# Kernel optimization log

Measured on AMD Instinct MI355X. Metric: run time of the kernel, lower is better.

Reference implementation:

```python
import jax, jax.numpy as jnp
import numpy as np

B, T, H = 2, 2048, 1024
EXPAND, N = 2, 16
DIN = H * EXPAND  # 2048
EPS = 1e-6


def rmsnorm(x, w):
    var = jnp.mean(x * x, axis=-1, keepdims=True)
    return x * jax.lax.rsqrt(var + EPS) * w


def setup_inputs() -> dict:
    key = jax.random.key(0)
    ks = jax.random.split(key, 9)
    s_h = 1.0 / np.sqrt(H)
    s_d = 1.0 / np.sqrt(DIN)
    return {
        "x": jax.random.normal(ks[0], (B, T, H), jnp.float32),
        "norm_w": jnp.ones((H,), jnp.float32),
        "in_proj_w": jax.random.normal(ks[1], (H, 2 * DIN), jnp.float32) * s_h,
        "A_proj_w": jax.random.normal(ks[2], (DIN, DIN), jnp.float32) * s_d,
        "A_proj_b": jax.random.normal(ks[3], (DIN,), jnp.float32) * 0.02,
        "A_base": jnp.log(jnp.arange(1, N + 1, dtype=jnp.float32)),
        "B_proj_w": jax.random.normal(ks[4], (DIN, N), jnp.float32) * s_d,
        "C_proj_w": jax.random.normal(ks[5], (DIN, N), jnp.float32) * s_d,
        "D": jnp.ones((DIN,), jnp.float32),
        "out_proj_w": jax.random.normal(ks[6], (DIN, H), jnp.float32) * s_d,
    }


def liquid_scan(x_in, a_mod, a_base, B_in, C_in):
    # x_in, a_mod: [B,T,DIN]; B_in, C_in: [B,T,N]; a_base: [N]
    def step(h, inp):
        a_t, b_t, c_t, x_t = inp  # [B,DIN], [B,N], [B,N], [B,DIN]
        # h: [B, DIN, N]
        h = (a_t[:, :, None] * a_base) * h + b_t[:, None, :] * x_t[:, :, None]
        y_t = jnp.einsum('bdn,bn->bd', h, c_t)
        return h, y_t

    h0 = jnp.zeros((x_in.shape[0], DIN, N), x_in.dtype)
    xs = (jnp.swapaxes(a_mod, 0, 1), jnp.swapaxes(B_in, 0, 1),
          jnp.swapaxes(C_in, 0, 1), jnp.swapaxes(x_in, 0, 1))
    _, ys = jax.lax.scan(step, h0, xs)  # ys: [T,B,DIN]
    return jnp.swapaxes(ys, 0, 1)


def reference(x, norm_w, in_proj_w, A_proj_w, A_proj_b, A_base, B_proj_w, C_proj_w, D, out_proj_w):
    residual = x
    xn = rmsnorm(x, norm_w)
    xz = xn @ in_proj_w                      # [B,T,2*DIN]
    x_in, z = jnp.split(xz, 2, axis=-1)
    x_in = jax.nn.silu(x_in)
    a_mod = jax.nn.sigmoid(x_in @ A_proj_w + A_proj_b)  # [B,T,DIN]
    a_base = jax.nn.sigmoid(A_base)                      # [N]
    B_in = x_in @ B_proj_w                               # [B,T,N]
    C_in = x_in @ C_proj_w                               # [B,T,N]
    y = liquid_scan(x_in, a_mod, a_base, B_in, C_in)     # [B,T,DIN]
    y = (y + D * x_in) * jax.nn.silu(z)
    return residual + y @ out_proj_w
```

## Files before the change

### kernel.cpp

```cpp
#include <hip/hip_runtime.h>
#include <hip/hip_fp16.h>
#include <cstdint>

#define B_    2
#define T_    2048
#define H_    1024
#define DIN_  2048
#define NS_   16
#define M_    (B_*T_)
#define NCHUNK 32
#define LCHUNK 64

using bf16x8 = __attribute__((ext_vector_type(8))) short;
using f32x4  = __attribute__((ext_vector_type(4))) float;

__device__ __forceinline__ unsigned short f2bf(float f) {
    union { float f; uint32_t u; } x; x.f = f;
    uint32_t u = x.u;
    uint32_t r = (u + 0x7fffu + ((u >> 16) & 1u)) >> 16;
    return (unsigned short)r;
}
__device__ __forceinline__ float bf2f(unsigned short h) {
    union { uint32_t u; float f; } x; x.u = ((uint32_t)h) << 16;
    return x.f;
}
__device__ __forceinline__ float sigm(float v) { return 1.0f / (1.0f + expf(-v)); }
__device__ __forceinline__ float silu(float v) { return v / (1.0f + expf(-v)); }

__device__ __forceinline__ void gload_lds16(const void* g, void* l) {
    __builtin_amdgcn_global_load_lds(
        (__attribute__((address_space(1))) void*)(void*)g,
        (__attribute__((address_space(3))) void*)l, 16, 0, 0);
}

__global__ __launch_bounds__(256)
void prep_weights(const float* __restrict__ in_proj, const float* __restrict__ A_proj,
                  const float* __restrict__ B_proj, const float* __restrict__ C_proj,
                  const float* __restrict__ out_proj,
                  unsigned short* __restrict__ inT, unsigned short* __restrict__ W2,
                  unsigned short* __restrict__ outT) {
    int bid = blockIdx.x;
    int tid = threadIdx.x;
    if (bid >= 10240) {
        int l = bid - 10240;
        const float* src = (l < 64) ? B_proj : C_proj;
        int rowoff = (l < 64) ? 2048 : 2064;
        int k0 = (l & 63) * 32;
        int r = tid >> 4, c = tid & 15;
#pragma unroll
        for (int rr = 0; rr < 32; rr += 16) {
            float v = src[(size_t)(k0 + r + rr) * 16 + c];
            W2[(size_t)(rowoff + c) * 2048 + (k0 + r + rr)] = f2bf(v);
        }
        return;
    }
    const float* src; unsigned short* dst; int K, N, l;
    if (bid < 4096)      { src = in_proj;  dst = inT;  K = 1024; N = 4096; l = bid; }
    else if (bid < 8192) { src = A_proj;   dst = W2;   K = 2048; N = 2048; l = bid - 4096; }
    else                 { src = out_proj; dst = outT; K = 2048; N = 1024; l = bid - 8192; }
    int ntiles = N >> 5;
    int n0 = (l % ntiles) * 32, k0 = (l / ntiles) * 32;
    __shared__ float tile[32][33];
    int tx = tid & 31, ty = tid >> 5;
#pragma unroll
    for (int i = 0; i < 32; i += 8)
        tile[ty + i][tx] = src[(size_t)(k0 + ty + i) * N + (n0 + tx)];
    __syncthreads();
    int sx = (tid & 15) * 2;
    int sy = tid >> 4;
#pragma unroll
    for (int i = 0; i < 32; i += 16) {
        int n = sy + i;
        float v0 = tile[sx][n], v1 = tile[sx + 1][n];
        size_t o = (size_t)(n0 + n) * K + (k0 + sx);
        *(ushort2*)&dst[o] = make_ushort2(f2bf(v0), f2bf(v1));
    }
}

__global__ __launch_bounds__(256)
void rmsnorm_bf(const float* __restrict__ x, const float* __restrict__ w,
                unsigned short* __restrict__ xh) {
    int row = blockIdx.x;
    int tid = threadIdx.x;
    const float4* xr = (const float4*)(x + (size_t)row * H_);
    float4 v = xr[tid];
    float ss = v.x * v.x + v.y * v.y + v.z * v.z + v.w * v.w;
#pragma unroll
    for (int o = 32; o > 0; o >>= 1) ss += __shfl_down(ss, o, 64);
    __shared__ float red[4];
    int lane = tid & 63, wv = tid >> 6;
    if (lane == 0) red[wv] = ss;
    __syncthreads();
    float tot = red[0] + red[1] + red[2] + red[3];
    float rstd = rsqrtf(tot / (float)H_ + 1e-6f);
    const float4* wr = (const float4*)w;
    float4 w4 = wr[tid];
    size_t o = (size_t)row * H_ + tid * 4;
    *(ushort4*)&xh[o] = make_ushort4(f2bf(v.x * rstd * w4.x), f2bf(v.y * rstd * w4.y),
                                     f2bf(v.z * rstd * w4.z), f2bf(v.w * rstd * w4.w));
}

template <int EPI, int TM>
__global__ __launch_bounds__(256)
void gemm_bf(const unsigned short* __restrict__ Aa, const unsigned short* __restrict__ Bw,
             int K,
             float* __restrict__ out0,
             unsigned short* __restrict__ oh, unsigned short* __restrict__ oz,
             const float* __restrict__ aux,
             __half* __restrict__ oha, float* __restrict__ obin, float* __restrict__ ocin) {
    constexpr int UA    = TM / 16;
    constexpr int UNITS = UA + 8;
    constexpr int SPW   = UNITS / 4;
    constexpr int WM    = TM / 32;
    __shared__ unsigned short sm[3][UNITS * 512];
    const int tid  = threadIdx.x;
    const int lane = tid & 63;
    const int wid  = tid >> 6;
    const int wm   = wid >> 1, wn = wid & 1;

    const int gx   = gridDim.x;
    const int nwg  = gx * gridDim.y;
    const int orig = blockIdx.y * gx + blockIdx.x;
    const int qq   = nwg >> 3;
    const int lid  = (orig & 7) * qq + (orig >> 3);
    const int bm   = (lid / gx) * TM;
    const int bn   = (lid % gx) * 128;

    const unsigned short* b0 = Aa + (size_t)bm * K;
    const unsigned short* b1 = Bw + (size_t)bn * K;
    const int srow  = lane >> 2;
    const int sgran = (lane & 3) ^ ((lane >> 3) & 3);
    const unsigned short* gp[SPW];
    int lofs[SPW];
#pragma unroll
    for (int j = 0; j < SPW; ++j) {
        int u = wid * SPW + j;
        const unsigned short* base = (u < UA) ? b0 : b1;
        int chunk = (u < UA) ? u : (u - UA);
        gp[j] = base + (size_t)(chunk * 16 + srow) * K + sgran * 8;
        lofs[j] = u * 512;
    }

    const int nk = K >> 5;
#pragma unroll
    for (int j = 0; j < SPW; ++j) gload_lds16(gp[j], &sm[0][lofs[j]]);
#pragma unroll
    for (int j = 0; j < SPW; ++j) gload_lds16(gp[j] + 32, &sm[1][lofs[j]]);

    const int fro = (lane & 15) * 32 + (((lane >> 4) ^ ((lane >> 1) & 3)) * 8);

    f32x4 acc[WM][4] = {};
    int bsel = 0;
    for (int kt = 0; kt < nk; ++kt) {
        if (kt + 1 < nk) {
            if constexpr (SPW == 4) asm volatile("s_waitcnt vmcnt(4)" ::: "memory");
            else                    asm volatile("s_waitcnt vmcnt(3)" ::: "memory");
        } else {
            asm volatile("s_waitcnt vmcnt(0)" ::: "memory");
        }
        __builtin_amdgcn_s_barrier();
        __builtin_amdgcn_sched_barrier(0);
        if (kt + 2 < nk) {
            int nb = bsel + 2; if (nb >= 3) nb -= 3;
#pragma unroll
            for (int j = 0; j < SPW; ++j)
                gload_lds16(gp[j] + (kt + 2) * 32, &sm[nb][lofs[j]]);
        }
        const unsigned short* sb = sm[bsel];
        bf16x8 af[WM], bf8[4];
#pragma unroll
        for (int m = 0; m < WM; ++m)
            af[m] = *(const bf16x8*)&sb[(wm * WM + m) * 512 + fro];
#pragma unroll
        for (int n = 0; n < 4; ++n)
            bf8[n] = *(const bf16x8*)&sb[(UA + wn * 4 + n) * 512 + fro];
#pragma unroll
        for (int m = 0; m < WM; ++m)
#pragma unroll
            for (int n = 0; n < 4; ++n)
                acc[m][n] = __builtin_amdgcn_mfma_f32_16x16x32_bf16(af[m], bf8[n], acc[m][n], 0, 0, 0);
        bsel += 1; if (bsel == 3) bsel = 0;
    }

#pragma unroll
    for (int m = 0; m < WM; ++m)
#pragma unroll
        for (int n = 0; n < 4; ++n) {
            int col  = bn + wn * 64 + n * 16 + (lane & 15);
            int row0 = bm + wm * (WM * 16) + m * 16 + ((lane >> 4) << 2);
#pragma unroll
            for (int r = 0; r < 4; ++r) {
                int row = row0 + r;
                float v = acc[m][n][r];
                if (EPI == 0) {
                    float s = silu(v);
                    if (col < DIN_) oh[(size_t)row * DIN_ + col] = f2bf(s);
                    else            oz[(size_t)row * DIN_ + (col - DIN_)] = f2bf(s);
                } else if (EPI == 1) {
                    if (col < 2048)      oha[(size_t)row * DIN_ + col] = __float2half(sigm(v + aux[col]));
                    else if (col < 2064) obin[(size_t)row * 16 + (col - 2048)] = v;
                    else if (col < 2080) ocin[(size_t)row * 16 + (col - 2064)] = v;
                } else {
                    out0[(size_t)row * H_ + col] = v + aux[(size_t)row * H_ + col];
                }
            }
        }
}

__global__ __launch_bounds__(256)
void scan_phase1(const __half* __restrict__ amod, const unsigned short* __restrict__ xh,
                 const float* __restrict__ Bin, const float* __restrict__ Abase,
                 float* __restrict__ P, float* __restrict__ S) {
    int d = blockIdx.x * 256 + threadIdx.x;
    int c = blockIdx.y;
    int b = blockIdx.z;
    float ab[16];
#pragma unroll
    for (int n = 0; n < 16; ++n) ab[n] = sigm(Abase[n]);
    float p[16], s[16];
#pragma unroll
    for (int n = 0; n < 16; ++n) { p[n] = 1.0f; s[n] = 0.0f; }
    int t0 = c * LCHUNK;
    for (int tt = 0; tt < LCHUNK; ++tt) {
        size_t mrow = (size_t)(b * T_ + t0 + tt);
        float a = __half2float(amod[mrow * DIN_ + d]);
        float x = bf2f(xh[mrow * DIN_ + d]);
        const float4* bt4 = (const float4*)(Bin + mrow * 16);
        float4 q0 = bt4[0], q1 = bt4[1], q2 = bt4[2], q3 = bt4[3];
        float bt[16];
        bt[0]=q0.x; bt[1]=q0.y; bt[2]=q0.z; bt[3]=q0.w;
        bt[4]=q1.x; bt[5]=q1.y; bt[6]=q1.z; bt[7]=q1.w;
        bt[8]=q2.x; bt[9]=q2.y; bt[10]=q2.z; bt[11]=q2.w;
        bt[12]=q3.x; bt[13]=q3.y; bt[14]=q3.z; bt[15]=q3.w;
#pragma unroll
        for (int n = 0; n < 16; ++n) {
            float dk = a * ab[n];
            p[n] *= dk;
            s[n] = fmaf(dk, s[n], bt[n] * x);
        }
    }
    size_t base = ((size_t)(b * NCHUNK + c) << 15) + (size_t)d * 16;
    float4* P4 = (float4*)(P + base);
    float4* S4 = (float4*)(S + base);
#pragma unroll
    for (int j = 0; j < 4; ++j) {
        P4[j] = make_float4(p[4*j], p[4*j+1], p[4*j+2], p[4*j+3]);
        S4[j] = make_float4(s[4*j], s[4*j+1], s[4*j+2], s[4*j+3]);
    }
}

__global__ __launch_bounds__(256)
void scan_phase2(const float* __restrict__ P, const float* __restrict__ S,
                 float* __restrict__ H0) {
    int idx = blockIdx.x * 256 + threadIdx.x;
    int b = idx >> 15;
    int dn = idx & 32767;
    float g = 0.f;
    for (int c = 0; c < NCHUNK; ++c) {
        size_t base = ((size_t)(b * NCHUNK + c) << 15) + dn;
        H0[base] = g;
        g = fmaf(P[base], g, S[base]);
    }
}

__global__ __launch_bounds__(256)
void scan_phase3(const __half* __restrict__ amod, const unsigned short* __restrict__ xh,
                 const float* __restrict__ Bin, const float* __restrict__ Cin,
                 const float* __restrict__ Abase, const float* __restrict__ H0,
                 const float* __restrict__ Dp, const unsigned short* __restrict__ szh,
                 unsigned short* __restrict__ yh) {
    int d = blockIdx.x * 256 + threadIdx.x;
    int c = blockIdx.y;
    int b = blockIdx.z;
    float ab[16];
#pragma unroll
    for (int n = 0; n < 16; ++n) ab[n] = sigm(Abase[n]);
    float h[16];
    size_t hbase = ((size_t)(b * NCHUNK + c) << 15) + (size_t)d * 16;
    const float4* H4 = (const float4*)(H0 + hbase);
#pragma unroll
    for (int j = 0; j < 4; ++j) {
        float4 t4 = H4[j];
        h[j*4] = t4.x; h[j*4+1] = t4.y; h[j*4+2] = t4.z; h[j*4+3] = t4.w;
    }
    float Dd = Dp[d];
    int t0 = c * LCHUNK;
    for (int tt = 0; tt < LCHUNK; ++tt) {
        size_t mrow = (size_t)(b * T_ + t0 + tt);
        float a = __half2float(amod[mrow * DIN_ + d]);
        float x = bf2f(xh[mrow * DIN_ + d]);
        const float4* bt4 = (const float4*)(Bin + mrow * 16);
        const float4* ct4 = (const float4*)(Cin + mrow * 16);
        float4 q0 = bt4[0], q1 = bt4[1], q2 = bt4[2], q3 = bt4[3];
        float4 r0 = ct4[0], r1 = ct4[1], r2 = ct4[2], r3 = ct4[3];
        float bt[16], ct[16];
        bt[0]=q0.x; bt[1]=q0.y; bt[2]=q0.z; bt[3]=q0.w;
        bt[4]=q1.x; bt[5]=q1.y; bt[6]=q1.z; bt[7]=q1.w;
        bt[8]=q2.x; bt[9]=q2.y; bt[10]=q2.z; bt[11]=q2.w;
        bt[12]=q3.x; bt[13]=q3.y; bt[14]=q3.z; bt[15]=q3.w;
        ct[0]=r0.x; ct[1]=r0.y; ct[2]=r0.z; ct[3]=r0.w;
        ct[4]=r1.x; ct[5]=r1.y; ct[6]=r1.z; ct[7]=r1.w;
        ct[8]=r2.x; ct[9]=r2.y; ct[10]=r2.z; ct[11]=r2.w;
        ct[12]=r3.x; ct[13]=r3.y; ct[14]=r3.z; ct[15]=r3.w;
        float y = 0.f;
#pragma unroll
        for (int n = 0; n < 16; ++n) {
            float dk = a * ab[n];
            h[n] = fmaf(dk, h[n], bt[n] * x);
            y = fmaf(h[n], ct[n], y);
        }
        float val = (y + Dd * x) * bf2f(szh[mrow * DIN_ + d]);
        yh[mrow * DIN_ + d] = f2bf(val);
    }
}

extern "C" void kernel_launch(void* const* d_in, const int* in_sizes, int n_in,
                              void* d_out, int out_size, void* d_ws, size_t ws_size,
                              hipStream_t stream) {
    const float* x          = (const float*)d_in[0];
    const float* norm_w     = (const float*)d_in[1];
    const float* in_proj_w  = (const float*)d_in[2];
    const float* A_proj_w   = (const float*)d_in[3];
    const float* A_proj_b   = (const float*)d_in[4];
    const float* A_base     = (const float*)d_in[5];
    const float* B_proj_w   = (const float*)d_in[6];
    const float* C_proj_w   = (const float*)d_in[7];
    const float* Dp         = (const float*)d_in[8];
    const float* out_proj_w = (const float*)d_in[9];
    float* out = (float*)d_out;

    char* ws = (char*)d_ws;
    size_t off = 0;
    auto alloc = [&](size_t bytes) -> char* {
        char* p = ws + off;
        off += (bytes + 255) & ~(size_t)255;
        return p;
    };
    unsigned short* inT  = (unsigned short*)alloc((size_t)4096 * 1024 * 2);
    unsigned short* W2   = (unsigned short*)alloc((size_t)2176 * 2048 * 2);
    unsigned short* outT = (unsigned short*)alloc((size_t)1024 * 2048 * 2);
    unsigned short* xnh  = (unsigned short*)alloc((size_t)M_ * H_ * 2);
    unsigned short* xinh = (unsigned short*)alloc((size_t)M_ * DIN_ * 2);
    unsigned short* szh  = (unsigned short*)alloc((size_t)M_ * DIN_ * 2);
    __half* amod  = (__half*)alloc((size_t)M_ * DIN_ * 2);
    float* Bin    = (float*)alloc((size_t)M_ * 16 * 4);
    float* Cin    = (float*)alloc((size_t)M_ * 16 * 4);
    float* Pw     = (float*)alloc((size_t)B_ * NCHUNK * DIN_ * NS_ * 4);
    float* Sw     = (float*)alloc((size_t)B_ * NCHUNK * DIN_ * NS_ * 4);
    float* H0w    = (float*)alloc((size_t)B_ * NCHUNK * DIN_ * NS_ * 4);
    unsigned short* yh = (unsigned short*)alloc((size_t)M_ * DIN_ * 2);
    (void)ws_size;

    prep_weights<<<10368, 256, 0, stream>>>(in_proj_w, A_proj_w, B_proj_w, C_proj_w,
                                            out_proj_w, inT, W2, outT);

    rmsnorm_bf<<<M_, 256, 0, stream>>>(x, norm_w, xnh);

    gemm_bf<0, 128><<<dim3(4096 / 128, M_ / 128), 256, 0, stream>>>(
        xnh, inT, 1024, nullptr, xinh, szh, nullptr, nullptr, nullptr, nullptr);

    gemm_bf<1, 128><<<dim3(17, M_ / 128), 256, 0, stream>>>(
        xinh, W2, 2048, nullptr, nullptr, nullptr, A_proj_b, amod, Bin, Cin);

    scan_phase1<<<dim3(DIN_ / 256, NCHUNK, B_), 256, 0, stream>>>(amod, xinh, Bin, A_base, Pw, Sw);
    scan_phase2<<<(B_ * DIN_ * NS_) / 256, 256, 0, stream>>>(Pw, Sw, H0w);
    scan_phase3<<<dim3(DIN_ / 256, NCHUNK, B_), 256, 0, stream>>>(
        amod, xinh, Bin, Cin, A_base, H0w, Dp, szh, yh);

    gemm_bf<2, 64><<<dim3(1024 / 128, M_ / 64), 256, 0, stream>>>(
        yh, outT, 2048, out, nullptr, nullptr, x, nullptr, nullptr, nullptr);
}
```

Baseline: 248.5 us.

## Use 256-row, 512-thread GEMM tiles for the in_proj and A/B/C projection GEMMs

```diff
diff --git a/kernel.cpp b/kernel.cpp
--- a/kernel.cpp
+++ b/kernel.cpp
@@ -41,6 +41,14 @@
                   unsigned short* __restrict__ outT) {
     int bid = blockIdx.x;
     int tid = threadIdx.x;
+    if (bid >= 10368) {
+        int l = bid - 10368;
+        uint4* p = (uint4*)&W2[(size_t)(2080 + l * 8) * 2048];
+        uint4 z = make_uint4(0, 0, 0, 0);
+#pragma unroll
+        for (int i = 0; i < 8; ++i) p[tid * 8 + i] = z;
+        return;
+    }
     if (bid >= 10240) {
         int l = bid - 10240;
         const float* src = (l < 64) ? B_proj : C_proj;
@@ -100,18 +108,116 @@
                                      f2bf(v.z * rstd * w4.z), f2bf(v.w * rstd * w4.w));
 }
 
+template <int EPI, int TN>
+__global__ __launch_bounds__(512, 2)
+void gemm_big(const unsigned short* __restrict__ Aa, const unsigned short* __restrict__ Bw,
+              int K,
+              unsigned short* __restrict__ oh, unsigned short* __restrict__ oz,
+              const float* __restrict__ aux,
+              __half* __restrict__ oha, float* __restrict__ obin, float* __restrict__ ocin) {
+    constexpr int UA  = 32;
+    constexpr int UB  = (TN / 16) * 2;
+    constexpr int U   = UA + UB;
+    constexpr int SPW = U / 8;
+    constexpr int WN  = TN / 64;
+    __shared__ unsigned short sm[2][U * 512];
+    const int tid  = threadIdx.x;
+    const int lane = tid & 63;
+    const int wid  = tid >> 6;
+    const int wm   = wid >> 2;
+    const int wn   = wid & 3;
+
+    const int gx   = gridDim.x;
+    const int nwg  = gx * gridDim.y;
+    const int orig = blockIdx.y * gx + blockIdx.x;
+    const int qq   = nwg >> 3;
+    const int lid  = (orig & 7) * qq + (orig >> 3);
+    const int bm   = (lid / gx) * 256;
+    const int bn   = (lid % gx) * TN;
+
+    const unsigned short* b0 = Aa + (size_t)bm * K;
+    const unsigned short* b1 = Bw + (size_t)bn * K;
+    const int srow  = lane >> 2;
+    const int sgran = (lane & 3) ^ ((lane >> 3) & 3);
+    const unsigned short* gp[SPW];
+    int lofs[SPW];
+#pragma unroll
+    for (int j = 0; j < SPW; ++j) {
+        int un = wid * SPW + j;
+        int rel = (un < UA) ? un : (un - UA);
+        const unsigned short* base = (un < UA) ? b0 : b1;
+        int chunk = rel >> 1, ks = rel & 1;
+        gp[j] = base + (size_t)(chunk * 16 + srow) * K + ks * 32 + sgran * 8;
+        lofs[j] = un * 512;
+    }
+
+    const int nt = K >> 6;
+#pragma unroll
+    for (int j = 0; j < SPW; ++j) gload_lds16(gp[j], &sm[0][lofs[j]]);
+
+    const int fro = (lane & 15) * 32 + (((lane >> 4) ^ ((lane >> 1) & 3)) * 8);
+
+    f32x4 acc[8][WN] = {};
+    for (int kt = 0; kt < nt; ++kt) {
+        asm volatile("s_waitcnt vmcnt(0)" ::: "memory");
+        __builtin_amdgcn_s_barrier();
+        __builtin_amdgcn_sched_barrier(0);
+        if (kt + 1 < nt) {
+#pragma unroll
+            for (int j = 0; j < SPW; ++j)
+                gload_lds16(gp[j] + (kt + 1) * 64, &sm[(kt + 1) & 1][lofs[j]]);
+        }
+        const unsigned short* sb = sm[kt & 1];
+#pragma unroll
+        for (int ks = 0; ks < 2; ++ks) {
+            bf16x8 af[8], bf8[WN];
+#pragma unroll
+            for (int mf = 0; mf < 8; ++mf)
+                af[mf] = *(const bf16x8*)&sb[((wm * 8 + mf) * 2 + ks) * 512 + fro];
+#pragma unroll
+            for (int nf = 0; nf < WN; ++nf)
+                bf8[nf] = *(const bf16x8*)&sb[(UA + (wn * WN + nf) * 2 + ks) * 512 + fro];
+            __builtin_amdgcn_s_setprio(1);
+#pragma unroll
+            for (int mf = 0; mf < 8; ++mf)
+#pragma unroll
+                for (int nf = 0; nf < WN; ++nf)
+                    acc[mf][nf] = __builtin_amdgcn_mfma_f32_16x16x32_bf16(af[mf], bf8[nf], acc[mf][nf], 0, 0, 0);
+            __builtin_amdgcn_s_setprio(0);
+        }
+    }
+
+#pragma unroll
+    for (int mf = 0; mf < 8; ++mf)
+#pragma unroll
+        for (int nf = 0; nf < WN; ++nf) {
+            int col  = bn + wn * (TN / 4) + nf * 16 + (lane & 15);
+            int row0 = bm + wm * 128 + mf * 16 + ((lane >> 4) << 2);
+#pragma unroll
+            for (int r = 0; r < 4; ++r) {
+                int row = row0 + r;
+                float v = acc[mf][nf][r];
+                if (EPI == 0) {
+                    float s = silu(v);
+                    if (col < DIN_) oh[(size_t)row * DIN_ + col] = f2bf(s);
+                    else            oz[(size_t)row * DIN_ + (col - DIN_)] = f2bf(s);
+                } else {
+                    if (col < 2048)      oha[(size_t)row * DIN_ + col] = __float2half(sigm(v + aux[col]));
+                    else if (col < 2064) obin[(size_t)row * 16 + (col - 2048)] = v;
+                    else if (col < 2080) ocin[(size_t)row * 16 + (col - 2064)] = v;
+                }
+            }
+        }
+}
+
 template <int EPI, int TM>
 __global__ __launch_bounds__(256)
 void gemm_bf(const unsigned short* __restrict__ Aa, const unsigned short* __restrict__ Bw,
-             int K,
-             float* __restrict__ out0,
-             unsigned short* __restrict__ oh, unsigned short* __restrict__ oz,
-             const float* __restrict__ aux,
-             __half* __restrict__ oha, float* __restrict__ obin, float* __restrict__ ocin) {
+             int K, float* __restrict__ out0, const float* __restrict__ aux) {
     constexpr int UA    = TM / 16;
     constexpr int UNITS = UA + 8;
     constexpr int SPW   = UNITS / 4;
-    constexpr int WM    = TM / 32;
+    constexpr int WM    = (TM * 2) / (4 * 16);
     __shared__ unsigned short sm[3][UNITS * 512];
     const int tid  = threadIdx.x;
     const int lane = tid & 63;
@@ -174,11 +280,13 @@
 #pragma unroll
         for (int n = 0; n < 4; ++n)
             bf8[n] = *(const bf16x8*)&sb[(UA + wn * 4 + n) * 512 + fro];
+        __builtin_amdgcn_s_setprio(1);
 #pragma unroll
         for (int m = 0; m < WM; ++m)
 #pragma unroll
             for (int n = 0; n < 4; ++n)
                 acc[m][n] = __builtin_amdgcn_mfma_f32_16x16x32_bf16(af[m], bf8[n], acc[m][n], 0, 0, 0);
+        __builtin_amdgcn_s_setprio(0);
         bsel += 1; if (bsel == 3) bsel = 0;
     }
 
@@ -191,18 +299,7 @@
 #pragma unroll
             for (int r = 0; r < 4; ++r) {
                 int row = row0 + r;
-                float v = acc[m][n][r];
-                if (EPI == 0) {
-                    float s = silu(v);
-                    if (col < DIN_) oh[(size_t)row * DIN_ + col] = f2bf(s);
-                    else            oz[(size_t)row * DIN_ + (col - DIN_)] = f2bf(s);
-                } else if (EPI == 1) {
-                    if (col < 2048)      oha[(size_t)row * DIN_ + col] = __float2half(sigm(v + aux[col]));
-                    else if (col < 2064) obin[(size_t)row * 16 + (col - 2048)] = v;
-                    else if (col < 2080) ocin[(size_t)row * 16 + (col - 2064)] = v;
-                } else {
-                    out0[(size_t)row * H_ + col] = v + aux[(size_t)row * H_ + col];
-                }
+                out0[(size_t)row * H_ + col] = acc[m][n][r] + aux[(size_t)row * H_ + col];
             }
         }
 }
@@ -351,16 +448,16 @@
     unsigned short* yh = (unsigned short*)alloc((size_t)M_ * DIN_ * 2);
     (void)ws_size;
 
-    prep_weights<<<10368, 256, 0, stream>>>(in_proj_w, A_proj_w, B_proj_w, C_proj_w,
+    prep_weights<<<10380, 256, 0, stream>>>(in_proj_w, A_proj_w, B_proj_w, C_proj_w,
                                             out_proj_w, inT, W2, outT);
 
     rmsnorm_bf<<<M_, 256, 0, stream>>>(x, norm_w, xnh);
 
-    gemm_bf<0, 128><<<dim3(4096 / 128, M_ / 128), 256, 0, stream>>>(
-        xnh, inT, 1024, nullptr, xinh, szh, nullptr, nullptr, nullptr, nullptr);
-
-    gemm_bf<1, 128><<<dim3(17, M_ / 128), 256, 0, stream>>>(
-        xinh, W2, 2048, nullptr, nullptr, nullptr, A_proj_b, amod, Bin, Cin);
+    gemm_big<0, 256><<<dim3(4096 / 256, M_ / 256), 512, 0, stream>>>(
+        xnh, inT, 1024, xinh, szh, nullptr, nullptr, nullptr, nullptr);
+
+    gemm_big<1, 128><<<dim3(2176 / 128, M_ / 256), 512, 0, stream>>>(
+        xinh, W2, 2048, nullptr, nullptr, A_proj_b, amod, Bin, Cin);
 
     scan_phase1<<<dim3(DIN_ / 256, NCHUNK, B_), 256, 0, stream>>>(amod, xinh, Bin, A_base, Pw, Sw);
     scan_phase2<<<(B_ * DIN_ * NS_) / 256, 256, 0, stream>>>(Pw, Sw, H0w);
@@ -368,5 +465,5 @@
         amod, xinh, Bin, Cin, A_base, H0w, Dp, szh, yh);
 
     gemm_bf<2, 64><<<dim3(1024 / 128, M_ / 64), 256, 0, stream>>>(
-        yh, outT, 2048, out, nullptr, nullptr, x, nullptr, nullptr, nullptr);
-}
+        yh, outT, 2048, out, x);
+}
```

After: 253.2 us. No clear change (+1.9%).

## Enlarge GEMM tiles to 512-thread blocks with K=64 steps; split B/C projection

Applied to the files above, without the earlier changes.

```diff
diff --git a/kernel.cpp b/kernel.cpp
--- a/kernel.cpp
+++ b/kernel.cpp
@@ -35,25 +35,11 @@
 
 __global__ __launch_bounds__(256)
 void prep_weights(const float* __restrict__ in_proj, const float* __restrict__ A_proj,
-                  const float* __restrict__ B_proj, const float* __restrict__ C_proj,
                   const float* __restrict__ out_proj,
                   unsigned short* __restrict__ inT, unsigned short* __restrict__ W2,
                   unsigned short* __restrict__ outT) {
     int bid = blockIdx.x;
     int tid = threadIdx.x;
-    if (bid >= 10240) {
-        int l = bid - 10240;
-        const float* src = (l < 64) ? B_proj : C_proj;
-        int rowoff = (l < 64) ? 2048 : 2064;
-        int k0 = (l & 63) * 32;
-        int r = tid >> 4, c = tid & 15;
-#pragma unroll
-        for (int rr = 0; rr < 32; rr += 16) {
-            float v = src[(size_t)(k0 + r + rr) * 16 + c];
-            W2[(size_t)(rowoff + c) * 2048 + (k0 + r + rr)] = f2bf(v);
-        }
-        return;
-    }
     const float* src; unsigned short* dst; int K, N, l;
     if (bid < 4096)      { src = in_proj;  dst = inT;  K = 1024; N = 4096; l = bid; }
     else if (bid < 8192) { src = A_proj;   dst = W2;   K = 2048; N = 2048; l = bid - 4096; }
@@ -100,23 +86,25 @@
                                      f2bf(v.z * rstd * w4.z), f2bf(v.w * rstd * w4.w));
 }
 
-template <int EPI, int TM>
-__global__ __launch_bounds__(256)
+template <int EPI, int TM, int TN, int MW, int NW>
+__global__ __launch_bounds__(512, 2)
 void gemm_bf(const unsigned short* __restrict__ Aa, const unsigned short* __restrict__ Bw,
              int K,
              float* __restrict__ out0,
              unsigned short* __restrict__ oh, unsigned short* __restrict__ oz,
-             const float* __restrict__ aux,
-             __half* __restrict__ oha, float* __restrict__ obin, float* __restrict__ ocin) {
-    constexpr int UA    = TM / 16;
-    constexpr int UNITS = UA + 8;
-    constexpr int SPW   = UNITS / 4;
-    constexpr int WM    = TM / 32;
+             const float* __restrict__ aux, __half* __restrict__ oha) {
+    constexpr int UA    = (TM / 16) * 2;
+    constexpr int UB    = (TN / 16) * 2;
+    constexpr int UNITS = UA + UB;
+    constexpr int SPW   = UNITS / 8;
+    constexpr int MF    = TM / MW / 16;
+    constexpr int NF    = TN / NW / 16;
     __shared__ unsigned short sm[3][UNITS * 512];
     const int tid  = threadIdx.x;
     const int lane = tid & 63;
     const int wid  = tid >> 6;
-    const int wm   = wid >> 1, wn = wid & 1;
+    const int wm   = wid / NW;
+    const int wn   = wid % NW;
 
     const int gx   = gridDim.x;
     const int nwg  = gx * gridDim.y;
@@ -124,7 +112,7 @@
     const int qq   = nwg >> 3;
     const int lid  = (orig & 7) * qq + (orig >> 3);
     const int bm   = (lid / gx) * TM;
-    const int bn   = (lid % gx) * 128;
+    const int bn   = (lid % gx) * TN;
 
     const unsigned short* b0 = Aa + (size_t)bm * K;
     const unsigned short* b1 = Bw + (size_t)bn * K;
@@ -135,76 +123,127 @@
 #pragma unroll
     for (int j = 0; j < SPW; ++j) {
         int u = wid * SPW + j;
+        int rel = (u < UA) ? u : (u - UA);
         const unsigned short* base = (u < UA) ? b0 : b1;
-        int chunk = (u < UA) ? u : (u - UA);
-        gp[j] = base + (size_t)(chunk * 16 + srow) * K + sgran * 8;
+        int chunk = rel >> 1, ks = rel & 1;
+        gp[j] = base + (size_t)(chunk * 16 + srow) * K + ks * 32 + sgran * 8;
         lofs[j] = u * 512;
     }
 
-    const int nk = K >> 5;
+    const int nt = K >> 6;
 #pragma unroll
     for (int j = 0; j < SPW; ++j) gload_lds16(gp[j], &sm[0][lofs[j]]);
 #pragma unroll
-    for (int j = 0; j < SPW; ++j) gload_lds16(gp[j] + 32, &sm[1][lofs[j]]);
+    for (int j = 0; j < SPW; ++j) gload_lds16(gp[j] + 64, &sm[1][lofs[j]]);
 
     const int fro = (lane & 15) * 32 + (((lane >> 4) ^ ((lane >> 1) & 3)) * 8);
 
-    f32x4 acc[WM][4] = {};
+    f32x4 acc[MF][NF] = {};
     int bsel = 0;
-    for (int kt = 0; kt < nk; ++kt) {
-        if (kt + 1 < nk) {
-            if constexpr (SPW == 4) asm volatile("s_waitcnt vmcnt(4)" ::: "memory");
-            else                    asm volatile("s_waitcnt vmcnt(3)" ::: "memory");
+    for (int kt = 0; kt < nt; ++kt) {
+        if (kt + 1 < nt) {
+            if constexpr (SPW == 6)      asm volatile("s_waitcnt vmcnt(6)" ::: "memory");
+            else if constexpr (SPW == 4) asm volatile("s_waitcnt vmcnt(4)" ::: "memory");
+            else                         asm volatile("s_waitcnt vmcnt(8)" ::: "memory");
         } else {
             asm volatile("s_waitcnt vmcnt(0)" ::: "memory");
         }
         __builtin_amdgcn_s_barrier();
         __builtin_amdgcn_sched_barrier(0);
-        if (kt + 2 < nk) {
+        if (kt + 2 < nt) {
             int nb = bsel + 2; if (nb >= 3) nb -= 3;
 #pragma unroll
             for (int j = 0; j < SPW; ++j)
-                gload_lds16(gp[j] + (kt + 2) * 32, &sm[nb][lofs[j]]);
+                gload_lds16(gp[j] + (size_t)(kt + 2) * 64, &sm[nb][lofs[j]]);
         }
         const unsigned short* sb = sm[bsel];
-        bf16x8 af[WM], bf8[4];
-#pragma unroll
-        for (int m = 0; m < WM; ++m)
-            af[m] = *(const bf16x8*)&sb[(wm * WM + m) * 512 + fro];
-#pragma unroll
-        for (int n = 0; n < 4; ++n)
-            bf8[n] = *(const bf16x8*)&sb[(UA + wn * 4 + n) * 512 + fro];
-#pragma unroll
-        for (int m = 0; m < WM; ++m)
-#pragma unroll
-            for (int n = 0; n < 4; ++n)
-                acc[m][n] = __builtin_amdgcn_mfma_f32_16x16x32_bf16(af[m], bf8[n], acc[m][n], 0, 0, 0);
+#pragma unroll
+        for (int ks = 0; ks < 2; ++ks) {
+            bf16x8 af[MF], bf8[NF];
+#pragma unroll
+            for (int mf = 0; mf < MF; ++mf)
+                af[mf] = *(const bf16x8*)&sb[((wm * MF + mf) * 2 + ks) * 512 + fro];
+#pragma unroll
+            for (int nf = 0; nf < NF; ++nf)
+                bf8[nf] = *(const bf16x8*)&sb[(UA + (wn * NF + nf) * 2 + ks) * 512 + fro];
+            __builtin_amdgcn_s_setprio(1);
+#pragma unroll
+            for (int mf = 0; mf < MF; ++mf)
+#pragma unroll
+                for (int nf = 0; nf < NF; ++nf)
+                    acc[mf][nf] = __builtin_amdgcn_mfma_f32_16x16x32_bf16(af[mf], bf8[nf], acc[mf][nf], 0, 0, 0);
+            __builtin_amdgcn_s_setprio(0);
+        }
         bsel += 1; if (bsel == 3) bsel = 0;
     }
 
 #pragma unroll
-    for (int m = 0; m < WM; ++m)
-#pragma unroll
-        for (int n = 0; n < 4; ++n) {
-            int col  = bn + wn * 64 + n * 16 + (lane & 15);
-            int row0 = bm + wm * (WM * 16) + m * 16 + ((lane >> 4) << 2);
+    for (int mf = 0; mf < MF; ++mf)
+#pragma unroll
+        for (int nf = 0; nf < NF; ++nf) {
+            int col  = bn + (wn * NF + nf) * 16 + (lane & 15);
+            int row0 = bm + (wm * MF + mf) * 16 + ((lane >> 4) << 2);
 #pragma unroll
             for (int r = 0; r < 4; ++r) {
                 int row = row0 + r;
-                float v = acc[m][n][r];
+                float v = acc[mf][nf][r];
                 if (EPI == 0) {
                     float s = silu(v);
                     if (col < DIN_) oh[(size_t)row * DIN_ + col] = f2bf(s);
                     else            oz[(size_t)row * DIN_ + (col - DIN_)] = f2bf(s);
                 } else if (EPI == 1) {
-                    if (col < 2048)      oha[(size_t)row * DIN_ + col] = __float2half(sigm(v + aux[col]));
-                    else if (col < 2064) obin[(size_t)row * 16 + (col - 2048)] = v;
-                    else if (col < 2080) ocin[(size_t)row * 16 + (col - 2064)] = v;
+                    oha[(size_t)row * DIN_ + col] = __float2half(sigm(v + aux[col]));
                 } else {
                     out0[(size_t)row * H_ + col] = v + aux[(size_t)row * H_ + col];
                 }
             }
         }
+}
+
+__global__ __launch_bounds__(256)
+void bc_proj(const unsigned short* __restrict__ xh,
+             const float* __restrict__ Bw, const float* __restrict__ Cw,
+             float* __restrict__ Bout, float* __restrict__ Cout) {
+    int m = blockIdx.x;
+    int tid = threadIdx.x;
+    float ab[16], ac[16];
+#pragma unroll
+    for (int i = 0; i < 16; ++i) { ab[i] = 0.f; ac[i] = 0.f; }
+    for (int k = tid; k < DIN_; k += 256) {
+        float x = bf2f(xh[(size_t)m * DIN_ + k]);
+        const float4* br = (const float4*)(Bw + (size_t)k * 16);
+        const float4* cr = (const float4*)(Cw + (size_t)k * 16);
+#pragma unroll
+        for (int j = 0; j < 4; ++j) {
+            float4 b4 = br[j], c4 = cr[j];
+            ab[j * 4 + 0] = fmaf(x, b4.x, ab[j * 4 + 0]);
+            ab[j * 4 + 1] = fmaf(x, b4.y, ab[j * 4 + 1]);
+            ab[j * 4 + 2] = fmaf(x, b4.z, ab[j * 4 + 2]);
+            ab[j * 4 + 3] = fmaf(x, b4.w, ab[j * 4 + 3]);
+            ac[j * 4 + 0] = fmaf(x, c4.x, ac[j * 4 + 0]);
+            ac[j * 4 + 1] = fmaf(x, c4.y, ac[j * 4 + 1]);
+            ac[j * 4 + 2] = fmaf(x, c4.z, ac[j * 4 + 2]);
+            ac[j * 4 + 3] = fmaf(x, c4.w, ac[j * 4 + 3]);
+        }
+    }
+    int lane = tid & 63, w = tid >> 6;
+#pragma unroll
+    for (int i = 0; i < 16; ++i)
+#pragma unroll
+        for (int o = 32; o > 0; o >>= 1) {
+            ab[i] += __shfl_down(ab[i], o, 64);
+            ac[i] += __shfl_down(ac[i], o, 64);
+        }
+    __shared__ float rb[4][16], rc[4][16];
+    if (lane == 0) {
+#pragma unroll
+        for (int i = 0; i < 16; ++i) { rb[w][i] = ab[i]; rc[w][i] = ac[i]; }
+    }
+    __syncthreads();
+    if (tid < 16) {
+        Bout[(size_t)m * 16 + tid] = rb[0][tid] + rb[1][tid] + rb[2][tid] + rb[3][tid];
+        Cout[(size_t)m * 16 + tid] = rc[0][tid] + rc[1][tid] + rc[2][tid] + rc[3][tid];
+    }
 }
 
 __global__ __launch_bounds__(256)
@@ -337,7 +376,7 @@
         return p;
     };
     unsigned short* inT  = (unsigned short*)alloc((size_t)4096 * 1024 * 2);
-    unsigned short* W2   = (unsigned short*)alloc((size_t)2176 * 2048 * 2);
+    unsigned short* W2   = (unsigned short*)alloc((size_t)2048 * 2048 * 2);
     unsigned short* outT = (unsigned short*)alloc((size_t)1024 * 2048 * 2);
     unsigned short* xnh  = (unsigned short*)alloc((size_t)M_ * H_ * 2);
     unsigned short* xinh = (unsigned short*)alloc((size_t)M_ * DIN_ * 2);
@@ -351,22 +390,23 @@
     unsigned short* yh = (unsigned short*)alloc((size_t)M_ * DIN_ * 2);
     (void)ws_size;
 
-    prep_weights<<<10368, 256, 0, stream>>>(in_proj_w, A_proj_w, B_proj_w, C_proj_w,
-                                            out_proj_w, inT, W2, outT);
+    prep_weights<<<10240, 256, 0, stream>>>(in_proj_w, A_proj_w, out_proj_w, inT, W2, outT);
 
     rmsnorm_bf<<<M_, 256, 0, stream>>>(x, norm_w, xnh);
 
-    gemm_bf<0, 128><<<dim3(4096 / 128, M_ / 128), 256, 0, stream>>>(
-        xnh, inT, 1024, nullptr, xinh, szh, nullptr, nullptr, nullptr, nullptr);
-
-    gemm_bf<1, 128><<<dim3(17, M_ / 128), 256, 0, stream>>>(
-        xinh, W2, 2048, nullptr, nullptr, nullptr, A_proj_b, amod, Bin, Cin);
+    gemm_bf<0, 256, 128, 4, 2><<<dim3(4096 / 128, M_ / 256), 512, 0, stream>>>(
+        xnh, inT, 1024, nullptr, xinh, szh, nullptr, nullptr);
+
+    gemm_bf<1, 256, 128, 4, 2><<<dim3(2048 / 128, M_ / 256), 512, 0, stream>>>(
+        xinh, W2, 2048, nullptr, nullptr, nullptr, A_proj_b, amod);
+
+    bc_proj<<<M_, 256, 0, stream>>>(xinh, B_proj_w, C_proj_w, Bin, Cin);
 
     scan_phase1<<<dim3(DIN_ / 256, NCHUNK, B_), 256, 0, stream>>>(amod, xinh, Bin, A_base, Pw, Sw);
     scan_phase2<<<(B_ * DIN_ * NS_) / 256, 256, 0, stream>>>(Pw, Sw, H0w);
     scan_phase3<<<dim3(DIN_ / 256, NCHUNK, B_), 256, 0, stream>>>(
         amod, xinh, Bin, Cin, A_base, H0w, Dp, szh, yh);
 
-    gemm_bf<2, 64><<<dim3(1024 / 128, M_ / 64), 256, 0, stream>>>(
-        yh, outT, 2048, out, nullptr, nullptr, x, nullptr, nullptr, nullptr);
-}
+    gemm_bf<2, 128, 128, 2, 4><<<dim3(1024 / 128, M_ / 128), 512, 0, stream>>>(
+        yh, outT, 2048, out, nullptr, nullptr, x, nullptr);
+}
```

Measured after the change: 294.5 us. 1.19x slower.
